# Optimization experiments

Hardware: AMD Instinct MI355X
Metric: run time of the kernel (lower is better)

## Reference

```python
import jax, jax.numpy as jnp
import numpy as np

N = 10000   # num nodes
E = 640000  # num edges
D_IN, D_HID, D_OUT = 128, 256, 128


def _cheb_layer(x, src, dst, dis, W0, W1, b):
    """PyG ChebConv with K=2, sym norm, lambda_max=2.0 (no edge weights):
    out = x @ W0 + (L_hat x) @ W1 + b, with L_hat = -D^{-1/2} A D^{-1/2}."""
    norm = -(dis[src] * dis[dst])                       # [E]
    msg = norm[:, None] * x[src]                        # [E, d]
    tx1 = jax.ops.segment_sum(msg, dst, num_segments=N)  # [N, d]
    return x @ W0 + tx1 @ W1 + b


def setup_inputs() -> dict:
    key = jax.random.key(0)
    ks = jax.random.split(key, 10)

    def glorot(k, fan_in, fan_out):
        s = jnp.sqrt(6.0 / (fan_in + fan_out))
        return jax.random.uniform(k, (fan_in, fan_out), jnp.float32, -s, s)

    x = jax.random.normal(ks[0], (N, D_IN), jnp.float32)
    edge_index = jax.random.randint(ks[1], (2, E), 0, N, jnp.int64)
    edge_type = jax.random.randint(ks[2], (E,), 0, 5, jnp.int64)
    return {
        "x": x,
        "edge_index": edge_index,
        "edge_type": edge_type,
        "W01": glorot(ks[3], D_IN, D_HID),
        "W11": glorot(ks[4], D_IN, D_HID),
        "b1": jnp.zeros((D_HID,), jnp.float32),
        "W02": glorot(ks[5], D_HID, D_HID),
        "W12": glorot(ks[6], D_HID, D_HID),
        "b2": jnp.zeros((D_HID,), jnp.float32),
        "W03": glorot(ks[7], D_HID, D_OUT),
        "W13": glorot(ks[8], D_HID, D_OUT),
        "b3": jnp.zeros((D_OUT,), jnp.float32),
    }


def reference(x, edge_index, edge_type, W01, W11, b1, W02, W12, b2, W03, W13, b3):
    # edge_type is unused by ChebConv (matches the original forward signature).
    src, dst = edge_index[0], edge_index[1]
    deg = jax.ops.segment_sum(jnp.ones((E,), x.dtype), src, num_segments=N)
    dis = jnp.where(deg > 0, jax.lax.rsqrt(jnp.maximum(deg, 1.0)), 0.0)
    # eval mode: dropout(p=0.4) is identity
    h = jax.nn.relu(_cheb_layer(x, src, dst, dis, W01, W11, b1))
    h = jax.nn.relu(_cheb_layer(h, src, dst, dis, W02, W12, b2))
    return _cheb_layer(h, src, dst, dis, W03, W13, b3)
```

## Files before the change

### kernel.cpp

```cpp
#include <hip/hip_runtime.h>

#define D_IN 128
#define D_HID 256
#define D_OUT 128
#define NBIN 10240
#define HB 256

typedef __attribute__((ext_vector_type(8))) unsigned short ushort8v;
typedef __attribute__((ext_vector_type(4))) unsigned short ushort4v;
typedef __attribute__((ext_vector_type(8))) short short8v;
typedef __attribute__((ext_vector_type(4))) float f32x4;
typedef __attribute__((ext_vector_type(2))) float f32x2;
typedef __attribute__((ext_vector_type(4))) unsigned int uint4v;

__device__ __forceinline__ unsigned short f2bf(float f) {
    unsigned u = __float_as_uint(f);
    unsigned r = (u + 0x7fffu + ((u >> 16) & 1u)) >> 16;
    return (unsigned short)r;
}
__device__ __forceinline__ float bf2f(unsigned short b) {
    return __uint_as_float((unsigned)b << 16);
}
__device__ __forceinline__ unsigned pk_f8x4(float a, float b, float c, float d) {
    int v = __builtin_amdgcn_cvt_pk_fp8_f32(a, b, 0, false);
    v = __builtin_amdgcn_cvt_pk_fp8_f32(c, d, v, true);
    return (unsigned)v;
}
__device__ __forceinline__ unsigned char f8_1(float a) {
    return (unsigned char)(__builtin_amdgcn_cvt_pk_fp8_f32(a, a, 0, false) & 0xff);
}


struct WtrArgs {
    const float* W[6];
    unsigned short* T[6];
    int K[6];
    int N[6];
    const float* xin;
    unsigned short* xout;
    unsigned char* xoutf8;
    int nElem;
};


__global__ __launch_bounds__(256) void k_hist(const int* __restrict__ src, const int* __restrict__ dst,
                                              unsigned short* __restrict__ psrc,
                                              unsigned short* __restrict__ pdst,
                                              int E, int EPB, WtrArgs wa) {
    __shared__ int h[NBIN];
    int b = blockIdx.x, t = threadIdx.x;
    if (blockIdx.y == 2) {
        const int starts[7] = {0, 32, 64, 128, 192, 224, 256};
        int m = 0;
        while (b >= starts[m + 1]) ++m;
        int local = b - starts[m];
        int K = wa.K[m], N = wa.N[m];
        int kt = K / 32;
        int k0 = (local % kt) * 32, n0 = (local / kt) * 32;
        float (*tile)[33] = (float(*)[33])h;
        int tx = t & 31, ty = t >> 5;
        const float* W = wa.W[m];
        unsigned short* Wt = wa.T[m];
        for (int i = ty; i < 32; i += 8) tile[i][tx] = W[(size_t)(k0 + i) * N + n0 + tx];
        __syncthreads();
        for (int i = ty; i < 32; i += 8) Wt[(size_t)(n0 + i) * K + k0 + tx] = f2bf(tile[tx][i]);
        int stride = HB * 256 * 4;
        for (int i = (b * 256 + t) * 4; i < wa.nElem; i += stride) {
            float4 v = *reinterpret_cast<const float4*>(&wa.xin[i]);
            ushort4v o;
            o[0] = f2bf(v.x); o[1] = f2bf(v.y); o[2] = f2bf(v.z); o[3] = f2bf(v.w);
            *reinterpret_cast<ushort4v*>(&wa.xout[i]) = o;
            *reinterpret_cast<unsigned*>(&wa.xoutf8[i]) = pk_f8x4(v.x, v.y, v.z, v.w);
        }
        return;
    }
    const int* arr = blockIdx.y ? dst : src;
    unsigned short* outp = blockIdx.y ? pdst : psrc;
    for (int i = t; i < NBIN; i += 256) h[i] = 0;
    __syncthreads();
    int beg = b * EPB, end = beg + EPB; if (end > E) end = E;
    for (int e = beg + t; e < end; e += 256)
        atomicAdd(&h[arr[e]], 1);
    __syncthreads();
    for (int i = t; i < NBIN; i += 256)
        outp[(size_t)b * NBIN + i] = (unsigned short)h[i];
}


__global__ __launch_bounds__(256) void k_colsum(const unsigned short* __restrict__ psrc,
                                                unsigned short* __restrict__ pdst,
                                                float* __restrict__ dis, int* __restrict__ cnt) {
    int bin = blockIdx.x * 256 + threadIdx.x;
    if (bin >= NBIN) return;
    int degs = 0;
    for (int b = 0; b < HB; ++b) degs += psrc[(size_t)b * NBIN + bin];
    int c = 0;
    for (int b = 0; b < HB; ++b) {
        int v = pdst[(size_t)b * NBIN + bin];
        pdst[(size_t)b * NBIN + bin] = (unsigned short)c;
        c += v;
    }
    dis[bin] = degs > 0 ? rsqrtf((float)degs) : 0.f;
    cnt[bin] = c;
}


__global__ void k_scan(const int* __restrict__ cnt, int* __restrict__ off, int n, int E) {
    __shared__ int sums[256];
    int t = threadIdx.x;
    int chunk = (n + 255) / 256;
    int beg = t * chunk;
    int end = beg + chunk; if (end > n) end = n;
    int s = 0;
    for (int i = beg; i < end; ++i) s += cnt[i];
    sums[t] = s;
    __syncthreads();
    if (t == 0) {
        int running = 0;
        for (int i = 0; i < 256; ++i) { int tmp = sums[i]; sums[i] = running; running += tmp; }
        off[n] = E;
    }
    __syncthreads();
    int pre = sums[t];
    for (int i = beg; i < end; ++i) { off[i] = pre; pre += cnt[i]; }
}


__global__ __launch_bounds__(256) void k_scatter2(const int* __restrict__ src, const int* __restrict__ dst,
                                                  const float* __restrict__ dis, const int* __restrict__ off,
                                                  const unsigned short* __restrict__ pfx,
                                                  unsigned* __restrict__ edges, int E, int EPB) {
    __shared__ int lcnt[NBIN];
    int b = blockIdx.x, t = threadIdx.x;
    for (int i = t; i < NBIN; i += 256) lcnt[i] = 0;
    __syncthreads();
    int beg = b * EPB, end = beg + EPB; if (end > E) end = E;
    const unsigned short* pf = pfx + (size_t)b * NBIN;
    for (int e = beg + t; e < end; e += 256) {
        int s = src[e], d = dst[e];
        int r = atomicAdd(&lcnt[d], 1);
        int pos = off[d] + (int)pf[d] + r;
        float nv = -(dis[s] * dis[d]);
        edges[pos] = ((unsigned)s << 16) | (unsigned)f2bf(nv);
    }
}


#define AGG_GATHER(eSet, vSet)                                                        \
    _Pragma("unroll")                                                                 \
    for (int u = 0; u < 8; ++u)                                                       \
        vSet[u] = *reinterpret_cast<const uint4v*>(&xf8[(size_t)(eSet[u] >> 16) * D + cbase]);

#define AGG_ACCUM(eSet, vSet)                                                         \
    _Pragma("unroll")                                                                 \
    for (int u = 0; u < 8; ++u) {                                                     \
        float nv = __uint_as_float(eSet[u] << 16);                                    \
        _Pragma("unroll")                                                             \
        for (int d = 0; d < 4; ++d) {                                                 \
            f32x2 lo = __builtin_amdgcn_cvt_pk_f32_fp8((int)vSet[u][d], false);       \
            f32x2 hi = __builtin_amdgcn_cvt_pk_f32_fp8((int)vSet[u][d], true);        \
            acc[4*d+0] += nv * lo[0]; acc[4*d+1] += nv * lo[1];                       \
            acc[4*d+2] += nv * hi[0]; acc[4*d+3] += nv * hi[1];                       \
        }                                                                             \
    }

#define AGG_ONE(e)                                                                    \
    {                                                                                 \
        float nv = __uint_as_float((e) << 16);                                        \
        uint4v v = *reinterpret_cast<const uint4v*>(&xf8[(size_t)((e) >> 16) * D + cbase]); \
        _Pragma("unroll")                                                             \
        for (int d = 0; d < 4; ++d) {                                                 \
            f32x2 lo = __builtin_amdgcn_cvt_pk_f32_fp8((int)v[d], false);             \
            f32x2 hi = __builtin_amdgcn_cvt_pk_f32_fp8((int)v[d], true);              \
            acc[4*d+0] += nv * lo[0]; acc[4*d+1] += nv * lo[1];                       \
            acc[4*d+2] += nv * hi[0]; acc[4*d+3] += nv * hi[1];                       \
        }                                                                             \
    }

template<int D, bool STBF, bool STF32, bool ADDB>
__global__ __launch_bounds__(256) void k_agg_f8(const int* __restrict__ off,
                                                const unsigned* __restrict__ edges,
                                                const unsigned char* __restrict__ xf8,
                                                unsigned short* __restrict__ outb,
                                                float* __restrict__ outf,
                                                const float* __restrict__ base, int n) {
    const int TPN = D / 16;
    const int NPB = 256 / TPN;
    int tid = threadIdx.x;
    int node = blockIdx.x * NPB + tid / TPN;
    if (node >= n) return;
    int cbase = (tid % TPN) * 16;
    int i = off[node], end = off[node + 1];
    float acc[16] = {};
    int nb = (end - i) >> 3;

    if (nb > 0) {
        unsigned e0[8], e1[8];
        uint4v v0[8], v1[8];
        #pragma unroll
        for (int u = 0; u < 8; ++u) e0[u] = edges[i + u];
        AGG_GATHER(e0, v0)
        int b = 1;
        for (; b + 1 < nb; b += 2) {
            int base1 = i + b * 8;
            #pragma unroll
            for (int u = 0; u < 8; ++u) e1[u] = edges[base1 + u];
            AGG_GATHER(e1, v1)
            AGG_ACCUM(e0, v0)
            int base0 = i + (b + 1) * 8;
            #pragma unroll
            for (int u = 0; u < 8; ++u) e0[u] = edges[base0 + u];
            AGG_GATHER(e0, v0)
            AGG_ACCUM(e1, v1)
        }
        if (b < nb) {
            int base1 = i + b * 8;
            #pragma unroll
            for (int u = 0; u < 8; ++u) e1[u] = edges[base1 + u];
            AGG_GATHER(e1, v1)
            AGG_ACCUM(e0, v0)
            AGG_ACCUM(e1, v1)
        } else {
            AGG_ACCUM(e0, v0)
        }
    }
    for (int t = i + nb * 8; t < end; ++t) {
        unsigned e = edges[t];
        AGG_ONE(e)
    }

    if (ADDB) {
        #pragma unroll
        for (int q = 0; q < 4; ++q) {
            float4 bq = *reinterpret_cast<const float4*>(&base[(size_t)node * D + cbase + q * 4]);
            acc[q*4+0] += bq.x; acc[q*4+1] += bq.y; acc[q*4+2] += bq.z; acc[q*4+3] += bq.w;
        }
    }
    if (STBF) {
        ushort8v ob0, ob1;
        #pragma unroll
        for (int j = 0; j < 8; ++j) { ob0[j] = f2bf(acc[j]); ob1[j] = f2bf(acc[8 + j]); }
        *reinterpret_cast<ushort8v*>(&outb[(size_t)node * D + cbase]) = ob0;
        *reinterpret_cast<ushort8v*>(&outb[(size_t)node * D + cbase + 8]) = ob1;
    }
    if (STF32) {
        #pragma unroll
        for (int q = 0; q < 4; ++q) {
            float4 o;
            o.x = acc[q*4+0]; o.y = acc[q*4+1]; o.z = acc[q*4+2]; o.w = acc[q*4+3];
            *reinterpret_cast<float4*>(&outf[(size_t)node * D + cbase + q * 4]) = o;
        }
    }
}


#define LDT 72

template<int K, bool RELU, bool HAS_B2, bool HAS_BIAS, bool ST_BF, bool ST_F8>
__global__ __launch_bounds__(256) void k_gemm_mfma(
        const unsigned short* __restrict__ A1, const unsigned short* __restrict__ W0t,
        const unsigned short* __restrict__ A2, const unsigned short* __restrict__ W1t,
        const float* __restrict__ bias,
        unsigned short* __restrict__ Cb, unsigned char* __restrict__ Cf8, int M, int N) {
    __shared__ unsigned short As[64 * LDT];
    __shared__ unsigned short Bs[128 * LDT];
    int tid = threadIdx.x, lane = tid & 63, wave = tid >> 6;
    int wm = wave >> 1, wn = wave & 1;
    int row0 = blockIdx.x * 64, col0 = blockIdx.y * 128;
    f32x4 acc[2][4];
    #pragma unroll
    for (int i = 0; i < 2; ++i)
        #pragma unroll
        for (int j = 0; j < 4; ++j)
            acc[i][j] = (f32x4){0.f, 0.f, 0.f, 0.f};

    int aRow = wm * 32 + (lane & 15);
    int bRow = wn * 64 + (lane & 15);
    int kOff = (lane >> 4) * 8;
    int sr = tid >> 2, sc = (tid & 3) * 8;
    int gra = row0 + sr; if (gra >= M) gra = M - 1;

    const int npass = HAS_B2 ? 2 : 1;
    for (int pass = 0; pass < npass; ++pass) {
        const unsigned short* A = pass ? A2 : A1;
        const unsigned short* W = pass ? W1t : W0t;
        for (int k0 = 0; k0 < K; k0 += 64) {
            #pragma unroll
            for (int h = 0; h < 2; ++h) {
                ushort8v va = *reinterpret_cast<const ushort8v*>(&A[(size_t)gra * K + k0 + sc + h * 32]);
                *reinterpret_cast<ushort8v*>(&As[sr * LDT + sc + h * 32]) = va;
            }
            #pragma unroll
            for (int g = 0; g < 2; ++g)
                #pragma unroll
                for (int h = 0; h < 2; ++h) {
                    int r = sr + g * 64;
                    ushort8v vb = *reinterpret_cast<const ushort8v*>(&W[(size_t)(col0 + r) * K + k0 + sc + h * 32]);
                    *reinterpret_cast<ushort8v*>(&Bs[r * LDT + sc + h * 32]) = vb;
                }
            __syncthreads();
            #pragma unroll
            for (int kk = 0; kk < 2; ++kk) {
                int ko = kOff + kk * 32;
                short8v a[2], bb[4];
                #pragma unroll
                for (int i = 0; i < 2; ++i)
                    a[i] = *reinterpret_cast<const short8v*>(&As[(aRow + i * 16) * LDT + ko]);
                #pragma unroll
                for (int i = 0; i < 4; ++i)
                    bb[i] = *reinterpret_cast<const short8v*>(&Bs[(bRow + i * 16) * LDT + ko]);
                #pragma unroll
                for (int mi = 0; mi < 2; ++mi)
                    #pragma unroll
                    for (int ni = 0; ni < 4; ++ni)
                        acc[mi][ni] = __builtin_amdgcn_mfma_f32_16x16x32_bf16(a[mi], bb[ni], acc[mi][ni], 0, 0, 0);
            }
            __syncthreads();
        }
    }

    int colBase = col0 + wn * 64 + (lane & 15);
    int rowSub = (lane >> 4) * 4;
    #pragma unroll
    for (int mi = 0; mi < 2; ++mi) {
        int rowF = row0 + wm * 32 + mi * 16 + rowSub;
        #pragma unroll
        for (int r = 0; r < 4; ++r) {
            int gr = rowF + r;
            if (gr < M) {
                #pragma unroll
                for (int ni = 0; ni < 4; ++ni) {
                    int gc = colBase + ni * 16;
                    float v = acc[mi][ni][r];
                    if (HAS_BIAS) v += bias[gc];
                    if (RELU)     v = fmaxf(v, 0.f);
                    if (ST_BF)    Cb[(size_t)gr * N + gc] = f2bf(v);
                    if (ST_F8)    Cf8[(size_t)gr * N + gc] = f8_1(v);
                }
            }
        }
    }
}


template<int K>
__global__ __launch_bounds__(256) void k_gemm_dual(
        const unsigned short* __restrict__ A1, const unsigned short* __restrict__ W03t,
        const unsigned short* __restrict__ W13t, const float* __restrict__ bias,
        float* __restrict__ part, unsigned char* __restrict__ y3f8, int M) {
    const int N = 128;
    __shared__ unsigned short As[64 * LDT];
    __shared__ unsigned short Bs[128 * LDT];
    int tid = threadIdx.x, lane = tid & 63, wave = tid >> 6;
    int wm = wave >> 1, wn = wave & 1;
    int row0 = blockIdx.x * 64;
    const unsigned short* W = blockIdx.y ? W13t : W03t;
    f32x4 acc[2][4];
    #pragma unroll
    for (int i = 0; i < 2; ++i)
        #pragma unroll
        for (int j = 0; j < 4; ++j)
            acc[i][j] = (f32x4){0.f, 0.f, 0.f, 0.f};

    int aRow = wm * 32 + (lane & 15);
    int bRow = wn * 64 + (lane & 15);
    int kOff = (lane >> 4) * 8;
    int sr = tid >> 2, sc = (tid & 3) * 8;
    int gra = row0 + sr; if (gra >= M) gra = M - 1;

    for (int k0 = 0; k0 < K; k0 += 64) {
        #pragma unroll
        for (int h = 0; h < 2; ++h) {
            ushort8v va = *reinterpret_cast<const ushort8v*>(&A1[(size_t)gra * K + k0 + sc + h * 32]);
            *reinterpret_cast<ushort8v*>(&As[sr * LDT + sc + h * 32]) = va;
        }
        #pragma unroll
        for (int g = 0; g < 2; ++g)
            #pragma unroll
            for (int h = 0; h < 2; ++h) {
                int r = sr + g * 64;
                ushort8v vb = *reinterpret_cast<const ushort8v*>(&W[(size_t)r * K + k0 + sc + h * 32]);
                *reinterpret_cast<ushort8v*>(&Bs[r * LDT + sc + h * 32]) = vb;
            }
        __syncthreads();
        #pragma unroll
        for (int kk = 0; kk < 2; ++kk) {
            int ko = kOff + kk * 32;
            short8v a[2], bb[4];
            #pragma unroll
            for (int i = 0; i < 2; ++i)
                a[i] = *reinterpret_cast<const short8v*>(&As[(aRow + i * 16) * LDT + ko]);
            #pragma unroll
            for (int i = 0; i < 4; ++i)
                bb[i] = *reinterpret_cast<const short8v*>(&Bs[(bRow + i * 16) * LDT + ko]);
            #pragma unroll
            for (int mi = 0; mi < 2; ++mi)
                #pragma unroll
                for (int ni = 0; ni < 4; ++ni)
                    acc[mi][ni] = __builtin_amdgcn_mfma_f32_16x16x32_bf16(a[mi], bb[ni], acc[mi][ni], 0, 0, 0);
        }
        __syncthreads();
    }

    int colBase = wn * 64 + (lane & 15);
    int rowSub = (lane >> 4) * 4;
    bool isPart = (blockIdx.y == 0);
    #pragma unroll
    for (int mi = 0; mi < 2; ++mi) {
        int rowF = row0 + wm * 32 + mi * 16 + rowSub;
        #pragma unroll
        for (int r = 0; r < 4; ++r) {
            int gr = rowF + r;
            if (gr < M) {
                #pragma unroll
                for (int ni = 0; ni < 4; ++ni) {
                    int gc = colBase + ni * 16;
                    float v = acc[mi][ni][r];
                    if (isPart) part[(size_t)gr * N + gc] = v + bias[gc];
                    else        y3f8[(size_t)gr * N + gc] = f8_1(v);
                }
            }
        }
    }
}


extern "C" void kernel_launch(void* const* d_in, const int* in_sizes, int n_in,
                              void* d_out, int out_size, void* d_ws, size_t ws_size,
                              hipStream_t stream) {
    const float* x   = (const float*)d_in[0];
    const int*   ei  = (const int*)d_in[1];
    const float* W01 = (const float*)d_in[3];
    const float* W11 = (const float*)d_in[4];
    const float* b1  = (const float*)d_in[5];
    const float* W02 = (const float*)d_in[6];
    const float* W12 = (const float*)d_in[7];
    const float* b2  = (const float*)d_in[8];
    const float* W03 = (const float*)d_in[9];
    const float* W13 = (const float*)d_in[10];
    const float* b3  = (const float*)d_in[11];
    float* out = (float*)d_out;

    const int n = in_sizes[0] / D_IN;
    const int E = in_sizes[1] / 2;
    const int* src = ei;
    const int* dst = ei + E;
    const int EPB = (E + HB - 1) / HB;

    char* wsb = (char*)d_ws;
    float* dis   = (float*)wsb;                   wsb += NBIN * 4;
    int*   cnt   = (int*)wsb;                     wsb += NBIN * 4;
    int*   off   = (int*)wsb;                     wsb += (NBIN + 16) * 4;
    unsigned short* psrc = (unsigned short*)wsb;  wsb += (size_t)HB * NBIN * 2;
    unsigned short* pdst = (unsigned short*)wsb;  wsb += (size_t)HB * NBIN * 2;
    unsigned* edges = (unsigned*)wsb;             wsb += (size_t)E * 4;
    unsigned short* txb  = (unsigned short*)wsb;  wsb += (size_t)n * D_HID * 2;
    float*          part = (float*)wsb;           wsb += (size_t)n * D_OUT * 4;
    unsigned short* x_bf = (unsigned short*)wsb;  wsb += (size_t)n * D_IN * 2;
    unsigned short* h1_bf = (unsigned short*)wsb; wsb += (size_t)n * D_HID * 2;
    unsigned short* h2_bf = (unsigned short*)wsb; wsb += (size_t)n * D_HID * 2;
    unsigned char* x_f8  = (unsigned char*)wsb;   wsb += (size_t)n * D_IN;
    unsigned char* h1_f8 = (unsigned char*)wsb;   wsb += (size_t)n * D_HID;
    unsigned char* y3_f8 = (unsigned char*)wsb;   wsb += (size_t)n * D_OUT;
    wsb = (char*)(((size_t)wsb + 255) & ~(size_t)255);
    unsigned short* W01t = (unsigned short*)wsb;  wsb += (size_t)D_IN  * D_HID * 2;
    unsigned short* W11t = (unsigned short*)wsb;  wsb += (size_t)D_IN  * D_HID * 2;
    unsigned short* W02t = (unsigned short*)wsb;  wsb += (size_t)D_HID * D_HID * 2;
    unsigned short* W12t = (unsigned short*)wsb;  wsb += (size_t)D_HID * D_HID * 2;
    unsigned short* W03t = (unsigned short*)wsb;  wsb += (size_t)D_HID * D_OUT * 2;
    unsigned short* W13t = (unsigned short*)wsb;  wsb += (size_t)D_HID * D_OUT * 2;

    const int gmx = (n + 63) / 64;
    const int ga128 = (n + 31) / 32;
    const int ga256 = (n + 15) / 16;

    WtrArgs wa;
    wa.W[0] = W01; wa.T[0] = W01t; wa.K[0] = D_IN;  wa.N[0] = D_HID;
    wa.W[1] = W11; wa.T[1] = W11t; wa.K[1] = D_IN;  wa.N[1] = D_HID;
    wa.W[2] = W02; wa.T[2] = W02t; wa.K[2] = D_HID; wa.N[2] = D_HID;
    wa.W[3] = W12; wa.T[3] = W12t; wa.K[3] = D_HID; wa.N[3] = D_HID;
    wa.W[4] = W03; wa.T[4] = W03t; wa.K[4] = D_HID; wa.N[4] = D_OUT;
    wa.W[5] = W13; wa.T[5] = W13t; wa.K[5] = D_HID; wa.N[5] = D_OUT;
    wa.xin = x; wa.xout = x_bf; wa.xoutf8 = x_f8; wa.nElem = n * D_IN;

    k_hist<<<dim3(HB, 3), 256, 0, stream>>>(src, dst, psrc, pdst, E, EPB, wa);
    k_colsum<<<NBIN / 256, 256, 0, stream>>>(psrc, pdst, dis, cnt);
    k_scan<<<1, 256, 0, stream>>>(cnt, off, n, E);
    k_scatter2<<<HB, 256, 0, stream>>>(src, dst, dis, off, pdst, edges, E, EPB);

    k_agg_f8<D_IN, true, false, false><<<ga128, 256, 0, stream>>>(
        off, edges, x_f8, txb, nullptr, nullptr, n);
    k_gemm_mfma<D_IN, true, true, true, true, true><<<dim3(gmx, D_HID / 128), 256, 0, stream>>>(
        x_bf, W01t, txb, W11t, b1, h1_bf, h1_f8, n, D_HID);

    k_agg_f8<D_HID, true, false, false><<<ga256, 256, 0, stream>>>(
        off, edges, h1_f8, txb, nullptr, nullptr, n);
    k_gemm_mfma<D_HID, true, true, true, true, false><<<dim3(gmx, D_HID / 128), 256, 0, stream>>>(
        h1_bf, W02t, txb, W12t, b2, h2_bf, nullptr, n, D_HID);

    k_gemm_dual<D_HID><<<dim3(gmx, 2), 256, 0, stream>>>(
        h2_bf, W03t, W13t, b3, part, y3_f8, n);
    k_agg_f8<D_OUT, false, true, true><<<ga128, 256, 0, stream>>>(
        off, edges, y3_f8, nullptr, out, part, n);
}
```

Measured before the change: 155.5 us.

## Fold scan into colsum via last-block pattern and fuse dual-GEMM passes

Removes the separate single-block scan launch by having the last k_colsum block (found via an atomic counter, reset in k_hist) compute the prefix offsets. The two-pass GEMM is restructured so both A/W pairs are staged into separate LDS buffers in one k-loop, halving the loop iterations and barriers. This raises LDS use per block, which may lower occupancy, and the atomic handoff adds a serialized tail to colsum.

```diff
diff --git a/kernel.cpp b/kernel.cpp
--- a/kernel.cpp
+++ b/kernel.cpp
@@ -46,10 +46,11 @@
 __global__ __launch_bounds__(256) void k_hist(const int* __restrict__ src, const int* __restrict__ dst,
                                               unsigned short* __restrict__ psrc,
                                               unsigned short* __restrict__ pdst,
-                                              int E, int EPB, WtrArgs wa) {
+                                              int E, int EPB, WtrArgs wa, int* __restrict__ done) {
     __shared__ int h[NBIN];
     int b = blockIdx.x, t = threadIdx.x;
     if (blockIdx.y == 2) {
+        if (b == 0 && t == 0) *done = 0;
         const int starts[7] = {0, 32, 64, 128, 192, 224, 256};
         int m = 0;
         while (b >= starts[m + 1]) ++m;
@@ -89,25 +90,31 @@
 
 __global__ __launch_bounds__(256) void k_colsum(const unsigned short* __restrict__ psrc,
                                                 unsigned short* __restrict__ pdst,
-                                                float* __restrict__ dis, int* __restrict__ cnt) {
-    int bin = blockIdx.x * 256 + threadIdx.x;
-    if (bin >= NBIN) return;
-    int degs = 0;
-    for (int b = 0; b < HB; ++b) degs += psrc[(size_t)b * NBIN + bin];
-    int c = 0;
-    for (int b = 0; b < HB; ++b) {
-        int v = pdst[(size_t)b * NBIN + bin];
-        pdst[(size_t)b * NBIN + bin] = (unsigned short)c;
-        c += v;
-    }
-    dis[bin] = degs > 0 ? rsqrtf((float)degs) : 0.f;
-    cnt[bin] = c;
-}
-
-
-__global__ void k_scan(const int* __restrict__ cnt, int* __restrict__ off, int n, int E) {
+                                                float* __restrict__ dis, int* __restrict__ cnt,
+                                                int* __restrict__ off, int* __restrict__ done,
+                                                int n, int E) {
+    int t = threadIdx.x;
+    int bin = blockIdx.x * 256 + t;
+    if (bin < NBIN) {
+        int degs = 0;
+        for (int b = 0; b < HB; ++b) degs += psrc[(size_t)b * NBIN + bin];
+        int c = 0;
+        for (int b = 0; b < HB; ++b) {
+            int v = pdst[(size_t)b * NBIN + bin];
+            pdst[(size_t)b * NBIN + bin] = (unsigned short)c;
+            c += v;
+        }
+        dis[bin] = degs > 0 ? rsqrtf((float)degs) : 0.f;
+        cnt[bin] = c;
+    }
+    __shared__ int isLast;
     __shared__ int sums[256];
-    int t = threadIdx.x;
+    __threadfence();
+    __syncthreads();
+    if (t == 0) isLast = (atomicAdd(done, 1) == (int)gridDim.x - 1) ? 1 : 0;
+    __syncthreads();
+    if (!isLast) return;
+    __threadfence();
     int chunk = (n + 255) / 256;
     int beg = t * chunk;
     int end = beg + chunk; if (end > n) end = n;
@@ -119,6 +126,7 @@
         int running = 0;
         for (int i = 0; i < 256; ++i) { int tmp = sums[i]; sums[i] = running; running += tmp; }
         off[n] = E;
+        *done = 0;
     }
     __syncthreads();
     int pre = sums[t];
@@ -256,14 +264,16 @@
 
 #define LDT 72
 
-template<int K, bool RELU, bool HAS_B2, bool HAS_BIAS, bool ST_BF, bool ST_F8>
-__global__ __launch_bounds__(256) void k_gemm_mfma(
+template<int K, bool RELU, bool ST_BF, bool ST_F8>
+__global__ __launch_bounds__(256) void k_gemm2(
         const unsigned short* __restrict__ A1, const unsigned short* __restrict__ W0t,
         const unsigned short* __restrict__ A2, const unsigned short* __restrict__ W1t,
         const float* __restrict__ bias,
         unsigned short* __restrict__ Cb, unsigned char* __restrict__ Cf8, int M, int N) {
-    __shared__ unsigned short As[64 * LDT];
-    __shared__ unsigned short Bs[128 * LDT];
+    __shared__ unsigned short As1[64 * LDT];
+    __shared__ unsigned short As2[64 * LDT];
+    __shared__ unsigned short Bs1[128 * LDT];
+    __shared__ unsigned short Bs2[128 * LDT];
     int tid = threadIdx.x, lane = tid & 63, wave = tid >> 6;
     int wm = wave >> 1, wn = wave & 1;
     int row0 = blockIdx.x * 64, col0 = blockIdx.y * 128;
@@ -280,43 +290,48 @@
     int sr = tid >> 2, sc = (tid & 3) * 8;
     int gra = row0 + sr; if (gra >= M) gra = M - 1;
 
-    const int npass = HAS_B2 ? 2 : 1;
-    for (int pass = 0; pass < npass; ++pass) {
-        const unsigned short* A = pass ? A2 : A1;
-        const unsigned short* W = pass ? W1t : W0t;
-        for (int k0 = 0; k0 < K; k0 += 64) {
+    for (int k0 = 0; k0 < K; k0 += 64) {
+        #pragma unroll
+        for (int h = 0; h < 2; ++h) {
+            ushort8v va1 = *reinterpret_cast<const ushort8v*>(&A1[(size_t)gra * K + k0 + sc + h * 32]);
+            ushort8v va2 = *reinterpret_cast<const ushort8v*>(&A2[(size_t)gra * K + k0 + sc + h * 32]);
+            *reinterpret_cast<ushort8v*>(&As1[sr * LDT + sc + h * 32]) = va1;
+            *reinterpret_cast<ushort8v*>(&As2[sr * LDT + sc + h * 32]) = va2;
+        }
+        #pragma unroll
+        for (int g = 0; g < 2; ++g)
             #pragma unroll
             for (int h = 0; h < 2; ++h) {
-                ushort8v va = *reinterpret_cast<const ushort8v*>(&A[(size_t)gra * K + k0 + sc + h * 32]);
-                *reinterpret_cast<ushort8v*>(&As[sr * LDT + sc + h * 32]) = va;
+                int r = sr + g * 64;
+                ushort8v vb1 = *reinterpret_cast<const ushort8v*>(&W0t[(size_t)(col0 + r) * K + k0 + sc + h * 32]);
+                ushort8v vb2 = *reinterpret_cast<const ushort8v*>(&W1t[(size_t)(col0 + r) * K + k0 + sc + h * 32]);
+                *reinterpret_cast<ushort8v*>(&Bs1[r * LDT + sc + h * 32]) = vb1;
+                *reinterpret_cast<ushort8v*>(&Bs2[r * LDT + sc + h * 32]) = vb2;
             }
-            #pragma unroll
-            for (int g = 0; g < 2; ++g)
+        __syncthreads();
+        #pragma unroll
+        for (int kk = 0; kk < 2; ++kk) {
+            int ko = kOff + kk * 32;
+            short8v a1[2], a2[2], b1[4], b2[4];
+            #pragma unroll
+            for (int i = 0; i < 2; ++i) {
+                a1[i] = *reinterpret_cast<const short8v*>(&As1[(aRow + i * 16) * LDT + ko]);
+                a2[i] = *reinterpret_cast<const short8v*>(&As2[(aRow + i * 16) * LDT + ko]);
+            }
+            #pragma unroll
+            for (int i = 0; i < 4; ++i) {
+                b1[i] = *reinterpret_cast<const short8v*>(&Bs1[(bRow + i * 16) * LDT + ko]);
+                b2[i] = *reinterpret_cast<const short8v*>(&Bs2[(bRow + i * 16) * LDT + ko]);
+            }
+            #pragma unroll
+            for (int mi = 0; mi < 2; ++mi)
                 #pragma unroll
-                for (int h = 0; h < 2; ++h) {
-                    int r = sr + g * 64;
-                    ushort8v vb = *reinterpret_cast<const ushort8v*>(&W[(size_t)(col0 + r) * K + k0 + sc + h * 32]);
-                    *reinterpret_cast<ushort8v*>(&Bs[r * LDT + sc + h * 32]) = vb;
+                for (int ni = 0; ni < 4; ++ni) {
+                    acc[mi][ni] = __builtin_amdgcn_mfma_f32_16x16x32_bf16(a1[mi], b1[ni], acc[mi][ni], 0, 0, 0);
+                    acc[mi][ni] = __builtin_amdgcn_mfma_f32_16x16x32_bf16(a2[mi], b2[ni], acc[mi][ni], 0, 0, 0);
                 }
-            __syncthreads();
-            #pragma unroll
-            for (int kk = 0; kk < 2; ++kk) {
-                int ko = kOff + kk * 32;
-                short8v a[2], bb[4];
-                #pragma unroll
-                for (int i = 0; i < 2; ++i)
-                    a[i] = *reinterpret_cast<const short8v*>(&As[(aRow + i * 16) * LDT + ko]);
-                #pragma unroll
-                for (int i = 0; i < 4; ++i)
-                    bb[i] = *reinterpret_cast<const short8v*>(&Bs[(bRow + i * 16) * LDT + ko]);
-                #pragma unroll
-                for (int mi = 0; mi < 2; ++mi)
-                    #pragma unroll
-                    for (int ni = 0; ni < 4; ++ni)
-                        acc[mi][ni] = __builtin_amdgcn_mfma_f32_16x16x32_bf16(a[mi], bb[ni], acc[mi][ni], 0, 0, 0);
-            }
-            __syncthreads();
-        }
+        }
+        __syncthreads();
     }
 
     int colBase = col0 + wn * 64 + (lane & 15);
@@ -331,11 +346,10 @@
                 #pragma unroll
                 for (int ni = 0; ni < 4; ++ni) {
                     int gc = colBase + ni * 16;
-                    float v = acc[mi][ni][r];
-                    if (HAS_BIAS) v += bias[gc];
-                    if (RELU)     v = fmaxf(v, 0.f);
-                    if (ST_BF)    Cb[(size_t)gr * N + gc] = f2bf(v);
-                    if (ST_F8)    Cf8[(size_t)gr * N + gc] = f8_1(v);
+                    float v = acc[mi][ni][r] + bias[gc];
+                    if (RELU)  v = fmaxf(v, 0.f);
+                    if (ST_BF) Cb[(size_t)gr * N + gc] = f2bf(v);
+                    if (ST_F8) Cf8[(size_t)gr * N + gc] = f8_1(v);
                 }
             }
         }
@@ -451,6 +465,7 @@
     float* dis   = (float*)wsb;                   wsb += NBIN * 4;
     int*   cnt   = (int*)wsb;                     wsb += NBIN * 4;
     int*   off   = (int*)wsb;                     wsb += (NBIN + 16) * 4;
+    int*   done  = (int*)wsb;                     wsb += 16;
     unsigned short* psrc = (unsigned short*)wsb;  wsb += (size_t)HB * NBIN * 2;
     unsigned short* pdst = (unsigned short*)wsb;  wsb += (size_t)HB * NBIN * 2;
     unsigned* edges = (unsigned*)wsb;             wsb += (size_t)E * 4;
@@ -483,19 +498,18 @@
     wa.W[5] = W13; wa.T[5] = W13t; wa.K[5] = D_HID; wa.N[5] = D_OUT;
     wa.xin = x; wa.xout = x_bf; wa.xoutf8 = x_f8; wa.nElem = n * D_IN;
 
-    k_hist<<<dim3(HB, 3), 256, 0, stream>>>(src, dst, psrc, pdst, E, EPB, wa);
-    k_colsum<<<NBIN / 256, 256, 0, stream>>>(psrc, pdst, dis, cnt);
-    k_scan<<<1, 256, 0, stream>>>(cnt, off, n, E);
+    k_hist<<<dim3(HB, 3), 256, 0, stream>>>(src, dst, psrc, pdst, E, EPB, wa, done);
+    k_colsum<<<NBIN / 256, 256, 0, stream>>>(psrc, pdst, dis, cnt, off, done, n, E);
     k_scatter2<<<HB, 256, 0, stream>>>(src, dst, dis, off, pdst, edges, E, EPB);
 
     k_agg_f8<D_IN, true, false, false><<<ga128, 256, 0, stream>>>(
         off, edges, x_f8, txb, nullptr, nullptr, n);
-    k_gemm_mfma<D_IN, true, true, true, true, true><<<dim3(gmx, D_HID / 128), 256, 0, stream>>>(
+    k_gemm2<D_IN, true, true, true><<<dim3(gmx, D_HID / 128), 256, 0, stream>>>(
         x_bf, W01t, txb, W11t, b1, h1_bf, h1_f8, n, D_HID);
 
     k_agg_f8<D_HID, true, false, false><<<ga256, 256, 0, stream>>>(
         off, edges, h1_f8, txb, nullptr, nullptr, n);
-    k_gemm_mfma<D_HID, true, true, true, true, false><<<dim3(gmx, D_HID / 128), 256, 0, stream>>>(
+    k_gemm2<D_HID, true, true, false><<<dim3(gmx, D_HID / 128), 256, 0, stream>>>(
         h1_bf, W02t, txb, W12t, b2, h2_bf, nullptr, n, D_HID);
 
     k_gemm_dual<D_HID><<<dim3(gmx, 2), 256, 0, stream>>>(
```

Result: slower. 158.9 us (+2.1%).

## Parallelize column prefix sum across warps and fuse scan via last-block pattern

Applied to the files above, without the earlier changes.

k_colsum now uses four wavefront groups per 64 bins, each summing a quarter of the 256 partial histograms. Cross-group prefixes are combined through shared memory, so each thread handles 64 rows instead of 256 and the grid has four times as many blocks. The separate single-block k_scan launch is folded into k_colsum: the last block to finish, found with an atomic counter, performs the global offset scan. This removes one kernel launch and shortens the serial per-thread loop, at the cost of a 64-entry register cache per thread and a global atomic plus threadfence.

```diff
diff --git a/kernel.cpp b/kernel.cpp
--- a/kernel.cpp
+++ b/kernel.cpp
@@ -46,10 +46,11 @@
 __global__ __launch_bounds__(256) void k_hist(const int* __restrict__ src, const int* __restrict__ dst,
                                               unsigned short* __restrict__ psrc,
                                               unsigned short* __restrict__ pdst,
-                                              int E, int EPB, WtrArgs wa) {
+                                              int E, int EPB, WtrArgs wa, int* __restrict__ done) {
     __shared__ int h[NBIN];
     int b = blockIdx.x, t = threadIdx.x;
     if (blockIdx.y == 2) {
+        if (b == 0 && t == 0) *done = 0;
         const int starts[7] = {0, 32, 64, 128, 192, 224, 256};
         int m = 0;
         while (b >= starts[m + 1]) ++m;
@@ -89,25 +90,51 @@
 
 __global__ __launch_bounds__(256) void k_colsum(const unsigned short* __restrict__ psrc,
                                                 unsigned short* __restrict__ pdst,
-                                                float* __restrict__ dis, int* __restrict__ cnt) {
-    int bin = blockIdx.x * 256 + threadIdx.x;
-    if (bin >= NBIN) return;
-    int degs = 0;
-    for (int b = 0; b < HB; ++b) degs += psrc[(size_t)b * NBIN + bin];
-    int c = 0;
-    for (int b = 0; b < HB; ++b) {
-        int v = pdst[(size_t)b * NBIN + bin];
+                                                float* __restrict__ dis, int* __restrict__ cnt,
+                                                int* __restrict__ off, int* __restrict__ done,
+                                                int n, int E) {
+    __shared__ int gsumS[4][64];
+    __shared__ int gsumD[4][64];
+    int t = threadIdx.x;
+    int lane = t & 63, g = t >> 6;
+    int bin = blockIdx.x * 64 + lane;
+
+    int vcache[64];
+    int sd = 0, ss = 0;
+    #pragma unroll
+    for (int k = 0; k < 64; ++k) {
+        int b = g * 64 + k;
+        vcache[k] = pdst[(size_t)b * NBIN + bin];
+        sd += vcache[k];
+        ss += psrc[(size_t)b * NBIN + bin];
+    }
+    gsumS[g][lane] = ss;
+    gsumD[g][lane] = sd;
+    __syncthreads();
+    int base = 0;
+    for (int gg = 0; gg < g; ++gg) base += gsumD[gg][lane];
+    int c = base;
+    #pragma unroll
+    for (int k = 0; k < 64; ++k) {
+        int b = g * 64 + k;
         pdst[(size_t)b * NBIN + bin] = (unsigned short)c;
-        c += v;
-    }
-    dis[bin] = degs > 0 ? rsqrtf((float)degs) : 0.f;
-    cnt[bin] = c;
-}
-
-
-__global__ void k_scan(const int* __restrict__ cnt, int* __restrict__ off, int n, int E) {
+        c += vcache[k];
+    }
+    if (g == 0) {
+        int degs = gsumS[0][lane] + gsumS[1][lane] + gsumS[2][lane] + gsumS[3][lane];
+        int ctot = gsumD[0][lane] + gsumD[1][lane] + gsumD[2][lane] + gsumD[3][lane];
+        dis[bin] = degs > 0 ? rsqrtf((float)degs) : 0.f;
+        cnt[bin] = ctot;
+    }
+
+    __shared__ int isLast;
     __shared__ int sums[256];
-    int t = threadIdx.x;
+    __threadfence();
+    __syncthreads();
+    if (t == 0) isLast = (atomicAdd(done, 1) == (int)gridDim.x - 1) ? 1 : 0;
+    __syncthreads();
+    if (!isLast) return;
+    __threadfence();
     int chunk = (n + 255) / 256;
     int beg = t * chunk;
     int end = beg + chunk; if (end > n) end = n;
@@ -119,6 +146,7 @@
         int running = 0;
         for (int i = 0; i < 256; ++i) { int tmp = sums[i]; sums[i] = running; running += tmp; }
         off[n] = E;
+        *done = 0;
     }
     __syncthreads();
     int pre = sums[t];
@@ -451,6 +479,7 @@
     float* dis   = (float*)wsb;                   wsb += NBIN * 4;
     int*   cnt   = (int*)wsb;                     wsb += NBIN * 4;
     int*   off   = (int*)wsb;                     wsb += (NBIN + 16) * 4;
+    int*   done  = (int*)wsb;                     wsb += 16;
     unsigned short* psrc = (unsigned short*)wsb;  wsb += (size_t)HB * NBIN * 2;
     unsigned short* pdst = (unsigned short*)wsb;  wsb += (size_t)HB * NBIN * 2;
     unsigned* edges = (unsigned*)wsb;             wsb += (size_t)E * 4;
@@ -483,9 +512,8 @@
     wa.W[5] = W13; wa.T[5] = W13t; wa.K[5] = D_HID; wa.N[5] = D_OUT;
     wa.xin = x; wa.xout = x_bf; wa.xoutf8 = x_f8; wa.nElem = n * D_IN;
 
-    k_hist<<<dim3(HB, 3), 256, 0, stream>>>(src, dst, psrc, pdst, E, EPB, wa);
-    k_colsum<<<NBIN / 256, 256, 0, stream>>>(psrc, pdst, dis, cnt);
-    k_scan<<<1, 256, 0, stream>>>(cnt, off, n, E);
+    k_hist<<<dim3(HB, 3), 256, 0, stream>>>(src, dst, psrc, pdst, E, EPB, wa, done);
+    k_colsum<<<NBIN / 64, 256, 0, stream>>>(psrc, pdst, dis, cnt, off, done, n, E);
     k_scatter2<<<HB, 256, 0, stream>>>(src, dst, dis, off, pdst, edges, E, EPB);
 
     k_agg_f8<D_IN, true, false, false><<<ga128, 256, 0, stream>>>(
```

Result: slower. 176.2 us (+13.3%).
